# Optimization experiments

Measured on AMD Instinct MI355X. Metric: run time of the kernel, lower is better.

Reference implementation:

```python
import jax, jax.numpy as jnp
import numpy as np

N = 131072   # total nodes
G = 4096     # graphs
E = 524288   # directed bond edges
C = 96       # hidden_channels
L = 8        # num_layers
F_IN = 64    # atom features
NT = 5       # targets


def setup_inputs() -> dict:
    key = jax.random.key(0)
    ks = jax.random.split(key, 32)
    def rn(k, shape, s=0.05):
        return jax.random.normal(k, shape, jnp.float32) * s
    inp = {
        'x': jax.random.normal(ks[0], (N, F_IN), jnp.float32),
        'edge_index': jax.random.randint(ks[1], (2, E), 0, N),
        'batch': jnp.sort(jax.random.randint(ks[2], (N,), 0, G)),
        'num_graphs': G,
        # atom encoder
        'enc_w': rn(ks[3], (F_IN, C)), 'enc_b': rn(ks[4], (C,)),
        # virtual node embedding + MLP (Linear->BN->SiLU->Linear)
        'vn_emb': rn(ks[5], (C,)),
        'vn_w1': rn(ks[6], (C, C)), 'vn_b1': rn(ks[7], (C,)),
        'vn_g1': 1.0 + rn(ks[8], (C,)), 'vn_be1': rn(ks[9], (C,)),
        'vn_w2': rn(ks[10], (C, C)), 'vn_b2': rn(ks[11], (C,)),
        # per-layer GIN MLP (Linear C->2C, BN, SiLU, Linear 2C->C) stacked over L
        'conv_w1': rn(ks[12], (L, C, 2 * C)), 'conv_b1': rn(ks[13], (L, 2 * C)),
        'conv_g1': 1.0 + rn(ks[14], (L, 2 * C)), 'conv_be1': rn(ks[15], (L, 2 * C)),
        'conv_w2': rn(ks[16], (L, 2 * C, C)), 'conv_b2': rn(ks[17], (L, C)),
        # per-layer outer BatchNorm
        'bn_g': 1.0 + rn(ks[18], (L, C)), 'bn_b': rn(ks[19], (L, C)),
        # head: C->C/2 (BN,SiLU) -> C/4 (BN,SiLU) -> NT
        'h_w1': rn(ks[20], (C, C // 2)), 'h_b1': rn(ks[21], (C // 2,)),
        'h_g1': 1.0 + rn(ks[22], (C // 2,)), 'h_be1': rn(ks[23], (C // 2,)),
        'h_w2': rn(ks[24], (C // 2, C // 4)), 'h_b2': rn(ks[25], (C // 4,)),
        'h_g2': 1.0 + rn(ks[26], (C // 4,)), 'h_be2': rn(ks[27], (C // 4,)),
        'h_w3': rn(ks[28], (C // 4, NT)), 'h_b3': rn(ks[29], (NT,)),
    }
    return inp


def _bn(x, g, b, eps=1e-5):
    # training-mode BatchNorm1d: biased batch variance (matches torch normalization)
    m = x.mean(0)
    v = x.var(0)
    return (x - m) * jax.lax.rsqrt(v + eps) * g + b


def reference(x, edge_index, batch, num_graphs, enc_w, enc_b, vn_emb,
              vn_w1, vn_b1, vn_g1, vn_be1, vn_w2, vn_b2,
              conv_w1, conv_b1, conv_g1, conv_be1, conv_w2, conv_b2,
              bn_g, bn_b,
              h_w1, h_b1, h_g1, h_be1, h_w2, h_b2, h_g2, h_be2, h_w3, h_b3):
    n = x.shape[0]
    gN = int(num_graphs)
    c = enc_w.shape[1]
    nl = conv_w1.shape[0]

    h = x @ enc_w + enc_b                                   # [n, C]
    vn = jnp.broadcast_to(vn_emb, (gN, c))                  # virtual node feats
    h = jnp.concatenate([h, vn], 0)                         # [n+gN, C]

    # vectorized virtual-node edges: (n+batch[i]) <-> i, both directions
    node_ids = jnp.arange(n, dtype=batch.dtype)
    vidx = n + batch
    src = jnp.concatenate([edge_index[0], vidx, node_ids])
    tgt = jnp.concatenate([edge_index[1], node_ids, vidx])
    total = n + gN

    for i in range(nl):
        # GINConv, eps=0: MLP(x + sum_neighbors)
        agg = jax.ops.segment_sum(h[src], tgt, num_segments=total)
        z = h + agg
        z = z @ conv_w1[i] + conv_b1[i]
        z = jax.nn.silu(_bn(z, conv_g1[i], conv_be1[i]))
        z = z @ conv_w2[i] + conv_b2[i]
        z = jax.nn.silu(_bn(z, bn_g[i], bn_b[i]))           # outer BN + SiLU (dropout=eval)
        h = z if i == 0 else h + z                          # residual after layer 0
        if i < nl - 1:
            v = h[n:]
            v = jax.nn.silu(_bn(v @ vn_w1 + vn_b1, vn_g1, vn_be1)) @ vn_w2 + vn_b2
            h = jnp.concatenate([h[:n], v], 0)

    hn = h[:n]
    sums = jax.ops.segment_sum(hn, batch, num_segments=gN)
    counts = jax.ops.segment_sum(jnp.ones((n,), hn.dtype), batch, num_segments=gN)
    pooled = sums / jnp.maximum(counts, 1.0)[:, None]       # global_mean_pool

    z = jax.nn.silu(_bn(pooled @ h_w1 + h_b1, h_g1, h_be1))
    z = jax.nn.silu(_bn(z @ h_w2 + h_b2, h_g2, h_be2))
    return z @ h_w3 + h_b3                                  # [G, 5]
```

## Files before the change

### kernel.cpp

```cpp
#include <hip/hip_runtime.h>
#include <hip/hip_bf16.h>

constexpr int N_   = 131072;
constexpr int G_   = 4096;
constexpr int E_   = 524288;
constexpr int C_   = 96;
constexpr int L_   = 8;
constexpr int FIN_ = 64;
constexpr int TOT_ = N_ + G_;

typedef __attribute__((ext_vector_type(8))) short short8v;
typedef __attribute__((ext_vector_type(4))) float f32x4;
using bf16 = __hip_bfloat16;

__device__ __forceinline__ float silu_f(float y) { return y / (1.f + __expf(-y)); }
__device__ __forceinline__ float toF(float x) { return x; }
__device__ __forceinline__ float toF(bf16 x)  { return __bfloat162float(x); }
__device__ __forceinline__ float bfbits2f(short s) {
  return __uint_as_float(((unsigned)(unsigned short)s) << 16);
}
__device__ __forceinline__ short f2bfbits(float f) {
  bf16 b = __float2bfloat16(f);
  return *reinterpret_cast<short*>(&b);
}
__device__ __forceinline__ void atomAddD(double* p, double v) { unsafeAtomicAdd(p, v); }


__global__ __launch_bounds__(256) void k_cast_x(const float* __restrict__ x, bf16* __restrict__ xb) {
  int idx = blockIdx.x * 256 + threadIdx.x;
  if (idx >= N_ * FIN_) return;
  xb[idx] = __float2bfloat16(x[idx]);
}

__global__ __launch_bounds__(256) void k_transT(const float* __restrict__ src, bf16* __restrict__ dst,
                                                int Kd, int Nd, int total) {
  int idx = blockIdx.x * 256 + threadIdx.x;
  if (idx >= total) return;
  int per = Kd * Nd;
  int i   = idx / per;
  int rem = idx - i * per;
  int k   = rem / Nd;
  int n   = rem - k * Nd;
  dst[(size_t)i * per + n * Kd + k] = __float2bfloat16(src[idx]);
}

__global__ __launch_bounds__(256) void k_deg_count(const int* __restrict__ tgt, int* __restrict__ deg) {
  int e = blockIdx.x * 256 + threadIdx.x;
  if (e >= E_) return;
  atomicAdd(&deg[tgt[e]], 1);
}

__global__ __launch_bounds__(256) void k_scan_local(const int* __restrict__ deg, int* __restrict__ lp,
                                                    int* __restrict__ bsum) {
  __shared__ int s[256];
  int t = threadIdx.x;
  int i = blockIdx.x * 256 + t;
  int v = deg[i];
  s[t] = v;
  __syncthreads();
  for (int off = 1; off < 256; off <<= 1) {
    int x = (t >= off) ? s[t - off] : 0;
    __syncthreads();
    s[t] += x;
    __syncthreads();
  }
  lp[i] = s[t] - v;
  if (t == 255) bsum[blockIdx.x] = s[255];
}

__global__ __launch_bounds__(512) void k_scan_bsum(const int* __restrict__ bsum, int* __restrict__ boff) {
  __shared__ int s[512];
  int t = threadIdx.x;
  int v = bsum[t];
  s[t] = v;
  __syncthreads();
  for (int off = 1; off < 512; off <<= 1) {
    int x = (t >= off) ? s[t - off] : 0;
    __syncthreads();
    s[t] += x;
    __syncthreads();
  }
  boff[t] = s[t] - v;
}

__global__ __launch_bounds__(256) void k_scan_add(int* __restrict__ rs, const int* __restrict__ boff) {
  int i = blockIdx.x * 256 + threadIdx.x;
  if (i > N_) return;
  if (i == N_) { rs[N_] = E_; return; }
  rs[i] += boff[i >> 8];
}

__global__ __launch_bounds__(256) void k_csr_fill(const int* __restrict__ src, const int* __restrict__ tgt,
                                                  const int* __restrict__ rs, int* __restrict__ cur,
                                                  int* __restrict__ ssrc) {
  int e = blockIdx.x * 256 + threadIdx.x;
  if (e >= E_) return;
  int t = tgt[e];
  int pos = atomicAdd(&cur[t], 1);
  ssrc[rs[t] + pos] = src[e];
}

__global__ __launch_bounds__(256) void k_gbounds(const int* __restrict__ batch, int* __restrict__ gstart) {
  int i = blockIdx.x * 256 + threadIdx.x;
  if (i > N_) return;
  if (i == N_) {
    int last = batch[N_ - 1];
    for (int g = last + 1; g <= G_; ++g) gstart[g] = N_;
    return;
  }
  int b  = batch[i];
  int bp = (i == 0) ? -1 : batch[i - 1];
  for (int g = bp + 1; g <= b; ++g) gstart[g] = i;
}

__global__ __launch_bounds__(192) void k_vnagg(const bf16* __restrict__ hb, const int* __restrict__ gstart,
                                               bf16* __restrict__ vna) {
  int slot = threadIdx.x / 24;
  int c4   = (threadIdx.x % 24) * 4;
  int g = blockIdx.x * 8 + slot;
  int i0 = gstart[g], i1 = gstart[g + 1];
  float s0 = 0.f, s1 = 0.f, s2 = 0.f, s3 = 0.f;
  for (int i = i0; i < i1; ++i) {
    short4 v = *(const short4*)((const short*)hb + (size_t)i * C_ + c4);
    s0 += bfbits2f(v.x); s1 += bfbits2f(v.y); s2 += bfbits2f(v.z); s3 += bfbits2f(v.w);
  }
  short4 o;
  o.x = f2bfbits(s0); o.y = f2bfbits(s1); o.z = f2bfbits(s2); o.w = f2bfbits(s3);
  *(short4*)((short*)vna + (size_t)g * C_ + c4) = o;
}

template <int K, int NOUT, bool INACT, bool OSTATS, typename OutT>
__global__ __launch_bounds__(512) void k_gemm(const bf16* __restrict__ A, const bf16* __restrict__ Wt,
                                              const float* __restrict__ bias,
                                              const double* __restrict__ stin,
                                              const float* __restrict__ gam, const float* __restrict__ bet,
                                              float Rin,
                                              OutT* __restrict__ out, double* __restrict__ stout) {
  constexpr int KK  = K / 32;
  constexpr int NT  = NOUT / 16;
  constexpr int UPR = K / 8;
  constexpr int LPR = UPR + 1;
  constexpr int LWB  = NOUT * LPR * 16;
  constexpr int ISCB = INACT ? 2 * K * 4 : 0;
  constexpr int SMB  = LWB + (ISCB > 0 ? ISCB : 1);
  __shared__ __align__(16) char smem[SMB];
  uint4* lw   = reinterpret_cast<uint4*>(smem);
  float* lsc  = reinterpret_cast<float*>(smem + LWB);
  float* lsh  = lsc + K;
  float* ssum = reinterpret_cast<float*>(smem);
  float* sqs  = ssum + 8 * NOUT;

  const uint4* wv = (const uint4*)Wt;
  for (int u = threadIdx.x; u < NOUT * UPR; u += 512) {
    int row = u / UPR, colu = u - row * UPR;
    lw[row * LPR + colu] = wv[u];
  }
  if (INACT) {
    for (int k = threadIdx.x; k < K; k += 512) {
      double mean = stin[k] / (double)Rin;
      double var  = stin[K + k] / (double)Rin - mean * mean;
      float sc = gam[k] * rsqrtf((float)var + 1e-5f);
      lsc[k] = sc;
      lsh[k] = bet[k] - (float)mean * sc;
    }
  }
  __syncthreads();

  int wave = threadIdx.x >> 6, lane = threadIdx.x & 63;
  int m0 = (blockIdx.x * 8 + wave) * 16;
  int lr = lane & 15, lg = lane >> 4;

  short8v a[KK];
  const short* Arow = (const short*)A + (size_t)(m0 + lr) * K + lg * 8;
#pragma unroll
  for (int kk = 0; kk < KK; ++kk) {
    short8v raw = *(const short8v*)(Arow + kk * 32);
    if (INACT) {
      int kbase = kk * 32 + lg * 8;
#pragma unroll
      for (int j = 0; j < 8; ++j) {
        float f = bfbits2f(raw[j]);
        f = silu_f(fmaf(f, lsc[kbase + j], lsh[kbase + j]));
        raw[j] = f2bfbits(f);
      }
    }
    a[kk] = raw;
  }

  f32x4 acc[NT];
#pragma unroll
  for (int nt = 0; nt < NT; ++nt) acc[nt] = (f32x4){0.f, 0.f, 0.f, 0.f};

#pragma unroll
  for (int nt = 0; nt < NT; ++nt) {
    const short* brow = (const short*)&lw[(nt * 16 + lr) * LPR] + lg * 8;
#pragma unroll
    for (int kk = 0; kk < KK; ++kk) {
      short8v b = *(const short8v*)(brow + kk * 32);
      acc[nt] = __builtin_amdgcn_mfma_f32_16x16x32_bf16(a[kk], b, acc[nt], 0, 0, 0);
    }
  }

  if (OSTATS) __syncthreads();

  int orow = m0 + (lg << 2);
#pragma unroll
  for (int nt = 0; nt < NT; ++nt) {
    int col = nt * 16 + lr;
    float bi = bias[col];
    float s = 0.f, q = 0.f;
#pragma unroll
    for (int r = 0; r < 4; ++r) {
      float y = acc[nt][r] + bi;
      float yb;
      if constexpr (sizeof(OutT) == 2) {
        bf16 b = __float2bfloat16(y);
        out[(size_t)(orow + r) * NOUT + col] = b;
        yb = __bfloat162float(b);
      } else {
        out[(size_t)(orow + r) * NOUT + col] = y;
        yb = y;
      }
      if (OSTATS) { s += yb; q += yb * yb; }
    }
    if (OSTATS) {
      s += __shfl_xor(s, 16, 64); s += __shfl_xor(s, 32, 64);
      q += __shfl_xor(q, 16, 64); q += __shfl_xor(q, 32, 64);
      if (lg == 0) { ssum[wave * NOUT + col] = s; sqs[wave * NOUT + col] = q; }
    }
  }
  if (OSTATS) {
    __syncthreads();
    int tid = threadIdx.x;
    if (tid < NOUT) {
      float s = 0.f, q = 0.f;
#pragma unroll
      for (int w = 0; w < 8; ++w) { s += ssum[w * NOUT + tid]; q += sqs[w * NOUT + tid]; }
      atomAddD(&stout[tid], (double)s);
      atomAddD(&stout[NOUT + tid], (double)q);
    }
  }
}

template <int K, int NOUT>
__global__ __launch_bounds__(512) void k_gemm_agg(const bf16* __restrict__ hb,
    const int* __restrict__ batch, const int* __restrict__ rs, const int* __restrict__ ssrc,
    const bf16* __restrict__ vna, const bf16* __restrict__ Wt, const float* __restrict__ bias,
    bf16* __restrict__ out, double* __restrict__ st) {
  constexpr int KK  = K / 32;
  constexpr int NT  = NOUT / 16;
  constexpr int UPR = K / 8;
  constexpr int LPR = UPR + 1;
  constexpr int LWB = NOUT * LPR * 16;
  __shared__ __align__(16) char smem[LWB];
  uint4* lw   = reinterpret_cast<uint4*>(smem);
  float* ssum = reinterpret_cast<float*>(smem);
  float* sqs  = ssum + 8 * NOUT;

  const uint4* wv = (const uint4*)Wt;
  for (int u = threadIdx.x; u < NOUT * UPR; u += 512) {
    int row = u / UPR, colu = u - row * UPR;
    lw[row * LPR + colu] = wv[u];
  }
  __syncthreads();

  int wave = threadIdx.x >> 6, lane = threadIdx.x & 63;
  int m0 = (blockIdx.x * 8 + wave) * 16;
  int lr = lane & 15, lg = lane >> 4;
  int row = m0 + lr;
  int koff = lg * 8;

  float av[KK * 8];
#pragma unroll
  for (int t = 0; t < KK * 8; ++t) av[t] = 0.f;

  auto addPtr = [&](const short* p) {
#pragma unroll
    for (int kk = 0; kk < KK; ++kk) {
      short8v v = *(const short8v*)(p + koff + kk * 32);
#pragma unroll
      for (int j = 0; j < 8; ++j) av[kk * 8 + j] += bfbits2f(v[j]);
    }
  };
  auto addPtr2 = [&](const short* p0, const short* p1) {
    short8v v0[KK], v1[KK];
#pragma unroll
    for (int kk = 0; kk < KK; ++kk) {
      v0[kk] = *(const short8v*)(p0 + koff + kk * 32);
      v1[kk] = *(const short8v*)(p1 + koff + kk * 32);
    }
#pragma unroll
    for (int kk = 0; kk < KK; ++kk)
#pragma unroll
      for (int j = 0; j < 8; ++j)
        av[kk * 8 + j] += bfbits2f(v0[kk][j]) + bfbits2f(v1[kk][j]);
  };
  auto hrow = [&](int r) { return (const short*)hb + (size_t)r * K; };

  if (row < N_) {
    addPtr2(hrow(row), hrow(N_ + batch[row]));
    int e = rs[row], e1 = rs[row + 1];
    for (; e + 2 <= e1; e += 2) addPtr2(hrow(ssrc[e]), hrow(ssrc[e + 1]));
    if (e < e1) addPtr(hrow(ssrc[e]));
  } else {
    addPtr2(hrow(row), (const short*)vna + (size_t)(row - N_) * K);
  }

  short8v a[KK];
#pragma unroll
  for (int kk = 0; kk < KK; ++kk)
#pragma unroll
    for (int j = 0; j < 8; ++j) a[kk][j] = f2bfbits(av[kk * 8 + j]);

  f32x4 acc[NT];
#pragma unroll
  for (int nt = 0; nt < NT; ++nt) acc[nt] = (f32x4){0.f, 0.f, 0.f, 0.f};

#pragma unroll
  for (int nt = 0; nt < NT; ++nt) {
    const short* brow = (const short*)&lw[(nt * 16 + lr) * LPR] + lg * 8;
#pragma unroll
    for (int kk = 0; kk < KK; ++kk) {
      short8v b = *(const short8v*)(brow + kk * 32);
      acc[nt] = __builtin_amdgcn_mfma_f32_16x16x32_bf16(a[kk], b, acc[nt], 0, 0, 0);
    }
  }

  __syncthreads();

  int orow = m0 + (lg << 2);
#pragma unroll
  for (int nt = 0; nt < NT; ++nt) {
    int col = nt * 16 + lr;
    float bi = bias[col];
    float s = 0.f, q = 0.f;
#pragma unroll
    for (int r = 0; r < 4; ++r) {
      float y = acc[nt][r] + bi;
      bf16 b = __float2bfloat16(y);
      out[(size_t)(orow + r) * NOUT + col] = b;
      float yb = __bfloat162float(b);
      s += yb; q += yb * yb;
    }
    s += __shfl_xor(s, 16, 64); s += __shfl_xor(s, 32, 64);
    q += __shfl_xor(q, 16, 64); q += __shfl_xor(q, 32, 64);
    if (lg == 0) { ssum[wave * NOUT + col] = s; sqs[wave * NOUT + col] = q; }
  }
  __syncthreads();
  int tid = threadIdx.x;
  if (tid < NOUT) {
    float s = 0.f, q = 0.f;
#pragma unroll
    for (int w = 0; w < 8; ++w) { s += ssum[w * NOUT + tid]; q += sqs[w * NOUT + tid]; }
    atomAddD(&st[tid], (double)s);
    atomAddD(&st[NOUT + tid], (double)q);
  }
}

__global__ __launch_bounds__(256) void k_fill_vn(bf16* __restrict__ hb, const float* __restrict__ vn) {
  int idx = blockIdx.x * 256 + threadIdx.x;
  if (idx >= G_ * C_) return;
  int c = idx % C_;
  hb[(size_t)N_ * C_ + idx] = __float2bfloat16(vn[c]);
}

template <int CC, typename T>
__global__ __launch_bounds__(256) void k_bnstats(const T* __restrict__ X, int R, double* __restrict__ st) {
  int c = threadIdx.x;
  float s = 0.f, q = 0.f;
  for (int r = blockIdx.x; r < R; r += gridDim.x) {
    float v = toF(X[(size_t)r * CC + c]);
    s += v;
    q += v * v;
  }
  atomAddD(&st[c], (double)s);
  atomAddD(&st[CC + c], (double)q);
}

template <int CC>
__global__ __launch_bounds__(256) void k_bnfin(const double* __restrict__ st, int R,
    const float* __restrict__ g, const float* __restrict__ be,
    float* __restrict__ scale, float* __restrict__ shift) {
  int c = threadIdx.x;
  if (c >= CC) return;
  double mean = st[c] / R;
  double var  = st[CC + c] / R - mean * mean;
  float sc = g[c] * rsqrtf((float)var + 1e-5f);
  scale[c] = sc;
  shift[c] = be[c] - (float)mean * sc;
}

__global__ __launch_bounds__(256) void k_update(const bf16* __restrict__ Z, bf16* __restrict__ hb,
    const double* __restrict__ st,
    const float* __restrict__ gam, const float* __restrict__ bet, int addResid) {
  __shared__ float lsc[C_], lsh[C_];
  if (threadIdx.x < C_) {
    int c = threadIdx.x;
    double mean = st[c] / (double)TOT_;
    double var  = st[C_ + c] / (double)TOT_ - mean * mean;
    float sc = gam[c] * rsqrtf((float)var + 1e-5f);
    lsc[c] = sc;
    lsh[c] = bet[c] - (float)mean * sc;
  }
  __syncthreads();
  int idx = blockIdx.x * 256 + threadIdx.x;
  if (idx >= TOT_ * C_ / 8) return;
  int cg = idx % (C_ / 8);
  int c0 = cg * 8;
  short8v zv = ((const short8v*)Z)[idx];
  short8v hv = ((const short8v*)hb)[idx];
  short8v o;
#pragma unroll
  for (int j = 0; j < 8; ++j) {
    float y = silu_f(fmaf(bfbits2f(zv[j]), lsc[c0 + j], lsh[c0 + j]));
    float hn = addResid ? (bfbits2f(hv[j]) + y) : y;
    o[j] = f2bfbits(hn);
  }
  ((short8v*)hb)[idx] = o;
}

template <int K, int M, bool INACT>
__global__ __launch_bounds__(256) void k_mm(const float* __restrict__ A,
    const float* __restrict__ W, const float* __restrict__ bias,
    const float* __restrict__ isc, const float* __restrict__ ish,
    float* __restrict__ out, int R) {
  int idx = blockIdx.x * 256 + threadIdx.x;
  if (idx >= R * M) return;
  int row = idx / M;
  int m   = idx - row * M;
  const float* ar = A + (size_t)row * K;
  float s = bias[m];
#pragma unroll 8
  for (int k = 0; k < K; ++k) {
    float a = ar[k];
    if (INACT) a = silu_f(fmaf(a, isc[k], ish[k]));
    s = fmaf(a, W[k * M + m], s);
  }
  out[idx] = s;
}

__global__ __launch_bounds__(256) void k_pool2(const bf16* __restrict__ hb, const int* __restrict__ gstart,
                                               float* __restrict__ pooled) {
  int idx = blockIdx.x * 256 + threadIdx.x;
  if (idx >= G_ * C_) return;
  int g = idx / C_;
  int c = idx - g * C_;
  int i0 = gstart[g], i1 = gstart[g + 1];
  float s = 0.f;
  for (int i = i0; i < i1; ++i) s += toF(hb[(size_t)i * C_ + c]);
  pooled[idx] = s / fmaxf((float)(i1 - i0), 1.0f);
}

static inline int gblk(long n) { return (int)((n + 255) / 256); }

extern "C" void kernel_launch(void* const* d_in, const int* in_sizes, int n_in,
                              void* d_out, int out_size, void* d_ws, size_t ws_size,
                              hipStream_t stream) {
  (void)in_sizes; (void)n_in; (void)out_size; (void)ws_size;
  const float* x       = (const float*)d_in[0];
  const int*   ei      = (const int*)d_in[1];
  const int*   batch   = (const int*)d_in[2];
  const float* enc_w   = (const float*)d_in[4];
  const float* enc_b   = (const float*)d_in[5];
  const float* vn_emb  = (const float*)d_in[6];
  const float* vn_w1   = (const float*)d_in[7];
  const float* vn_b1   = (const float*)d_in[8];
  const float* vn_g1   = (const float*)d_in[9];
  const float* vn_be1  = (const float*)d_in[10];
  const float* vn_w2   = (const float*)d_in[11];
  const float* vn_b2   = (const float*)d_in[12];
  const float* conv_w1 = (const float*)d_in[13];
  const float* conv_b1 = (const float*)d_in[14];
  const float* conv_g1 = (const float*)d_in[15];
  const float* conv_be1= (const float*)d_in[16];
  const float* conv_w2 = (const float*)d_in[17];
  const float* conv_b2 = (const float*)d_in[18];
  const float* bn_g    = (const float*)d_in[19];
  const float* bn_b    = (const float*)d_in[20];
  const float* h_w1    = (const float*)d_in[21];
  const float* h_b1    = (const float*)d_in[22];
  const float* h_g1    = (const float*)d_in[23];
  const float* h_be1   = (const float*)d_in[24];
  const float* h_w2    = (const float*)d_in[25];
  const float* h_b2    = (const float*)d_in[26];
  const float* h_g2    = (const float*)d_in[27];
  const float* h_be2   = (const float*)d_in[28];
  const float* h_w3    = (const float*)d_in[29];
  const float* h_b3    = (const float*)d_in[30];
  float* out = (float*)d_out;

  const int* e_src = ei;
  const int* e_tgt = ei + E_;

  char* p = (char*)d_ws;
  auto alloc = [&](size_t bytes) -> char* {
    char* r = p;
    p += (bytes + 15) & ~size_t(15);
    return r;
  };
  bf16*   hbf    = (bf16*)  alloc((size_t)TOT_ * C_ * 2);
  bf16*   vna    = (bf16*)  alloc((size_t)G_ * C_ * 2);
  bf16*   vtb    = (bf16*)  alloc((size_t)G_ * C_ * 2);
  float*  pooled = (float*) alloc((size_t)G_ * C_ * 4);
  float*  t1     = (float*) alloc((size_t)G_ * 48 * 4);
  float*  t2     = (float*) alloc((size_t)G_ * 24 * 4);
  float*  scale1 = (float*) alloc(256 * 4);
  float*  shift1 = (float*) alloc(256 * 4);
  float*  scale2 = (float*) alloc(256 * 4);
  float*  shift2 = (float*) alloc(256 * 4);
  double* stbuf  = (double*)alloc((size_t)26 * 384 * 8);
  bf16*   z1     = (bf16*)  alloc((size_t)TOT_ * 2 * C_ * 2);
  bf16*   z2     = (bf16*)  alloc((size_t)TOT_ * C_ * 2);
  bf16*   xb     = (bf16*)  alloc((size_t)N_ * FIN_ * 2);
  bf16*   encwT  = (bf16*)  alloc((size_t)C_ * FIN_ * 2);
  bf16*   w1T    = (bf16*)  alloc((size_t)L_ * 2 * C_ * C_ * 2);
  bf16*   w2T    = (bf16*)  alloc((size_t)L_ * C_ * 2 * C_ * 2);
  bf16*   vnw1T  = (bf16*)  alloc((size_t)C_ * C_ * 2);
  bf16*   vnw2T  = (bf16*)  alloc((size_t)C_ * C_ * 2);
  int*    deg    = (int*)   alloc((size_t)N_ * 4);
  int*    cur    = (int*)   alloc((size_t)N_ * 4);
  int*    rs     = (int*)   alloc((size_t)(N_ + 1) * 4);
  int*    bsum   = (int*)   alloc(512 * 4);
  int*    boff   = (int*)   alloc(512 * 4);
  int*    ssrc   = (int*)   alloc((size_t)E_ * 4);
  int*    gstart = (int*)   alloc((size_t)(G_ + 1) * 4);

  auto ST = [&](int i) { return stbuf + (size_t)i * 384; };

  k_cast_x<<<gblk((long)N_ * FIN_), 256, 0, stream>>>(x, xb);
  k_transT<<<gblk((long)FIN_ * C_), 256, 0, stream>>>(enc_w, encwT, FIN_, C_, FIN_ * C_);
  k_transT<<<gblk((long)L_ * C_ * 2 * C_), 256, 0, stream>>>(conv_w1, w1T, C_, 2 * C_, L_ * C_ * 2 * C_);
  k_transT<<<gblk((long)L_ * 2 * C_ * C_), 256, 0, stream>>>(conv_w2, w2T, 2 * C_, C_, L_ * 2 * C_ * C_);
  k_transT<<<gblk((long)C_ * C_), 256, 0, stream>>>(vn_w1, vnw1T, C_, C_, C_ * C_);
  k_transT<<<gblk((long)C_ * C_), 256, 0, stream>>>(vn_w2, vnw2T, C_, C_, C_ * C_);

  hipMemsetAsync(deg, 0, (size_t)N_ * 4, stream);
  hipMemsetAsync(cur, 0, (size_t)N_ * 4, stream);
  hipMemsetAsync(stbuf, 0, (size_t)26 * 384 * 8, stream);
  k_deg_count<<<gblk(E_), 256, 0, stream>>>(e_tgt, deg);
  k_scan_local<<<N_ / 256, 256, 0, stream>>>(deg, rs, bsum);
  k_scan_bsum<<<1, 512, 0, stream>>>(bsum, boff);
  k_scan_add<<<gblk(N_ + 1), 256, 0, stream>>>(rs, boff);
  k_csr_fill<<<gblk(E_), 256, 0, stream>>>(e_src, e_tgt, rs, cur, ssrc);
  k_gbounds<<<gblk(N_ + 1), 256, 0, stream>>>(batch, gstart);

  k_gemm<FIN_, C_, false, false, bf16><<<N_ / 128, 512, 0, stream>>>(
      xb, encwT, enc_b, nullptr, nullptr, nullptr, 1.f, hbf, nullptr);
  k_fill_vn<<<gblk((long)G_ * C_), 256, 0, stream>>>(hbf, vn_emb);

  for (int i = 0; i < L_; ++i) {
    const bf16*  wt1 = w1T + (size_t)i * 2 * C_ * C_;
    const bf16*  wt2 = w2T + (size_t)i * C_ * 2 * C_;
    const float* b1  = conv_b1 + (size_t)i * 2 * C_;
    const float* g1  = conv_g1 + (size_t)i * 2 * C_;
    const float* be1 = conv_be1+ (size_t)i * 2 * C_;
    const float* b2  = conv_b2 + (size_t)i * C_;
    const float* bg  = bn_g    + (size_t)i * C_;
    const float* bb  = bn_b    + (size_t)i * C_;

    k_vnagg<<<G_ / 8, 192, 0, stream>>>(hbf, gstart, vna);

    k_gemm_agg<C_, 2 * C_><<<TOT_ / 128, 512, 0, stream>>>(
        hbf, batch, rs, ssrc, vna, wt1, b1, z1, ST(i));

    k_gemm<2 * C_, C_, true, true, bf16><<<TOT_ / 128, 512, 0, stream>>>(
        z1, wt2, b2, ST(i), g1, be1, (float)TOT_, z2, ST(8 + i));

    k_update<<<(int)((long)TOT_ * C_ / 8 / 256), 256, 0, stream>>>(z2, hbf, ST(8 + i), bg, bb, i > 0);

    if (i < L_ - 1) {
      k_gemm<C_, C_, false, true, bf16><<<G_ / 128, 512, 0, stream>>>(
          hbf + (size_t)N_ * C_, vnw1T, vn_b1, nullptr, nullptr, nullptr, 1.f, vtb, ST(16 + i));
      k_gemm<C_, C_, true, false, bf16><<<G_ / 128, 512, 0, stream>>>(
          vtb, vnw2T, vn_b2, ST(16 + i), vn_g1, vn_be1, (float)G_,
          hbf + (size_t)N_ * C_, nullptr);
    }
  }

  k_pool2<<<gblk((long)G_ * C_), 256, 0, stream>>>(hbf, gstart, pooled);

  k_mm<C_, 48, false><<<gblk((long)G_ * 48), 256, 0, stream>>>(
      pooled, h_w1, h_b1, nullptr, nullptr, t1, G_);
  k_bnstats<48, float><<<64, 48, 0, stream>>>(t1, G_, ST(23));
  k_bnfin<48><<<1, 48, 0, stream>>>(ST(23), G_, h_g1, h_be1, scale1, shift1);

  k_mm<48, 24, true><<<gblk((long)G_ * 24), 256, 0, stream>>>(
      t1, h_w2, h_b2, scale1, shift1, t2, G_);
  k_bnstats<24, float><<<64, 24, 0, stream>>>(t2, G_, ST(24));
  k_bnfin<24><<<1, 24, 0, stream>>>(ST(24), G_, h_g2, h_be2, scale2, shift2);

  k_mm<24, 5, true><<<gblk((long)G_ * 5), 256, 0, stream>>>(
      t2, h_w3, h_b3, scale2, shift2, out, G_);
}
```

Baseline: 1.267 ms.

## Fuse x cast into encoder GEMM, merge weight transposes, add nontemporal accesses

The separate fp32-to-bf16 cast of x is removed, and the encoder GEMM now reads fp32 x directly and converts it in registers. The six weight-transpose launches are merged into one k_prep kernel. Nontemporal loads and stores are added on the z1/z2 streaming paths, and the barrier after weight staging is moved after the A-tile global loads so they overlap the LDS fill. Together these cut launches and one full pass over x, at the cost of reading fp32 x at twice the bytes inside the GEMM.

Result: slower. 1.440 ms (+13.6%).

```diff
diff --git a/kernel.cpp b/kernel.cpp
--- a/kernel.cpp
+++ b/kernel.cpp
@@ -25,23 +25,27 @@
 }
 __device__ __forceinline__ void atomAddD(double* p, double v) { unsafeAtomicAdd(p, v); }
 
-
-__global__ __launch_bounds__(256) void k_cast_x(const float* __restrict__ x, bf16* __restrict__ xb) {
+static inline int gblk(long n) { return (int)((n + 255) / 256); }
+
+__global__ __launch_bounds__(256) void k_prep(const float* __restrict__ enc_w,
+    const float* __restrict__ conv_w1, const float* __restrict__ conv_w2,
+    const float* __restrict__ vn_w1, const float* __restrict__ vn_w2,
+    bf16* __restrict__ encwT, bf16* __restrict__ w1T, bf16* __restrict__ w2T,
+    bf16* __restrict__ vnw1T, bf16* __restrict__ vnw2T) {
   int idx = blockIdx.x * 256 + threadIdx.x;
-  if (idx >= N_ * FIN_) return;
-  xb[idx] = __float2bfloat16(x[idx]);
-}
-
-__global__ __launch_bounds__(256) void k_transT(const float* __restrict__ src, bf16* __restrict__ dst,
-                                                int Kd, int Nd, int total) {
-  int idx = blockIdx.x * 256 + threadIdx.x;
-  if (idx >= total) return;
+  const float* src; bf16* dst; int Kd, Nd, local;
+  if (idx < 6144)        { src = enc_w;   dst = encwT; Kd = 64;  Nd = 96;  local = idx; }
+  else if (idx < 153600) { src = conv_w1; dst = w1T;   Kd = 96;  Nd = 192; local = idx - 6144; }
+  else if (idx < 301056) { src = conv_w2; dst = w2T;   Kd = 192; Nd = 96;  local = idx - 153600; }
+  else if (idx < 310272) { src = vn_w1;   dst = vnw1T; Kd = 96;  Nd = 96;  local = idx - 301056; }
+  else if (idx < 319488) { src = vn_w2;   dst = vnw2T; Kd = 96;  Nd = 96;  local = idx - 310272; }
+  else return;
   int per = Kd * Nd;
-  int i   = idx / per;
-  int rem = idx - i * per;
+  int i   = local / per;
+  int rem = local - i * per;
   int k   = rem / Nd;
   int n   = rem - k * Nd;
-  dst[(size_t)i * per + n * Kd + k] = __float2bfloat16(src[idx]);
+  dst[(size_t)i * per + n * Kd + k] = __float2bfloat16(src[local]);
 }
 
 __global__ __launch_bounds__(256) void k_deg_count(const int* __restrict__ tgt, int* __restrict__ deg) {
@@ -129,8 +133,8 @@
   *(short4*)((short*)vna + (size_t)g * C_ + c4) = o;
 }
 
-template <int K, int NOUT, bool INACT, bool OSTATS, typename OutT>
-__global__ __launch_bounds__(512) void k_gemm(const bf16* __restrict__ A, const bf16* __restrict__ Wt,
+template <int K, int NOUT, bool INACT, bool OSTATS, bool AF32, bool NTA, bool NTO, typename OutT>
+__global__ __launch_bounds__(512) void k_gemm(const void* __restrict__ Aptr, const bf16* __restrict__ Wt,
                                               const float* __restrict__ bias,
                                               const double* __restrict__ stin,
                                               const float* __restrict__ gam, const float* __restrict__ bet,
@@ -164,27 +168,45 @@
       lsh[k] = bet[k] - (float)mean * sc;
     }
   }
-  __syncthreads();
 
   int wave = threadIdx.x >> 6, lane = threadIdx.x & 63;
   int m0 = (blockIdx.x * 8 + wave) * 16;
   int lr = lane & 15, lg = lane >> 4;
 
   short8v a[KK];
-  const short* Arow = (const short*)A + (size_t)(m0 + lr) * K + lg * 8;
-#pragma unroll
-  for (int kk = 0; kk < KK; ++kk) {
-    short8v raw = *(const short8v*)(Arow + kk * 32);
-    if (INACT) {
+  if constexpr (AF32) {
+    const float* Arow = (const float*)Aptr + (size_t)(m0 + lr) * K + lg * 8;
+#pragma unroll
+    for (int kk = 0; kk < KK; ++kk) {
+      float4 f0 = *(const float4*)(Arow + kk * 32);
+      float4 f1 = *(const float4*)(Arow + kk * 32 + 4);
+      a[kk][0] = f2bfbits(f0.x); a[kk][1] = f2bfbits(f0.y);
+      a[kk][2] = f2bfbits(f0.z); a[kk][3] = f2bfbits(f0.w);
+      a[kk][4] = f2bfbits(f1.x); a[kk][5] = f2bfbits(f1.y);
+      a[kk][6] = f2bfbits(f1.z); a[kk][7] = f2bfbits(f1.w);
+    }
+  } else {
+    const short* Arow = (const short*)Aptr + (size_t)(m0 + lr) * K + lg * 8;
+#pragma unroll
+    for (int kk = 0; kk < KK; ++kk) {
+      if constexpr (NTA) a[kk] = __builtin_nontemporal_load((const short8v*)(Arow + kk * 32));
+      else               a[kk] = *(const short8v*)(Arow + kk * 32);
+    }
+  }
+
+  __syncthreads();
+
+  if (INACT) {
+#pragma unroll
+    for (int kk = 0; kk < KK; ++kk) {
       int kbase = kk * 32 + lg * 8;
 #pragma unroll
       for (int j = 0; j < 8; ++j) {
-        float f = bfbits2f(raw[j]);
+        float f = bfbits2f(a[kk][j]);
         f = silu_f(fmaf(f, lsc[kbase + j], lsh[kbase + j]));
-        raw[j] = f2bfbits(f);
+        a[kk][j] = f2bfbits(f);
       }
     }
-    a[kk] = raw;
   }
 
   f32x4 acc[NT];
@@ -213,12 +235,15 @@
     for (int r = 0; r < 4; ++r) {
       float y = acc[nt][r] + bi;
       float yb;
+      size_t off = (size_t)(orow + r) * NOUT + col;
       if constexpr (sizeof(OutT) == 2) {
-        bf16 b = __float2bfloat16(y);
-        out[(size_t)(orow + r) * NOUT + col] = b;
-        yb = __bfloat162float(b);
+        short bits = f2bfbits(y);
+        if constexpr (NTO) __builtin_nontemporal_store(bits, (short*)out + off);
+        else               ((short*)out)[off] = bits;
+        yb = bfbits2f(bits);
       } else {
-        out[(size_t)(orow + r) * NOUT + col] = y;
+        if constexpr (NTO) __builtin_nontemporal_store(y, (float*)out + off);
+        else               ((float*)out)[off] = y;
         yb = y;
       }
       if (OSTATS) { s += yb; q += yb * yb; }
@@ -262,7 +287,6 @@
     int row = u / UPR, colu = u - row * UPR;
     lw[row * LPR + colu] = wv[u];
   }
-  __syncthreads();
 
   int wave = threadIdx.x >> 6, lane = threadIdx.x & 63;
   int m0 = (blockIdx.x * 8 + wave) * 16;
@@ -312,6 +336,8 @@
 #pragma unroll
     for (int j = 0; j < 8; ++j) a[kk][j] = f2bfbits(av[kk * 8 + j]);
 
+  __syncthreads();
+
   f32x4 acc[NT];
 #pragma unroll
   for (int nt = 0; nt < NT; ++nt) acc[nt] = (f32x4){0.f, 0.f, 0.f, 0.f};
@@ -337,9 +363,9 @@
 #pragma unroll
     for (int r = 0; r < 4; ++r) {
       float y = acc[nt][r] + bi;
-      bf16 b = __float2bfloat16(y);
-      out[(size_t)(orow + r) * NOUT + col] = b;
-      float yb = __bfloat162float(b);
+      short bits = f2bfbits(y);
+      __builtin_nontemporal_store(bits, (short*)out + (size_t)(orow + r) * NOUT + col);
+      float yb = bfbits2f(bits);
       s += yb; q += yb * yb;
     }
     s += __shfl_xor(s, 16, 64); s += __shfl_xor(s, 32, 64);
@@ -407,7 +433,7 @@
   if (idx >= TOT_ * C_ / 8) return;
   int cg = idx % (C_ / 8);
   int c0 = cg * 8;
-  short8v zv = ((const short8v*)Z)[idx];
+  short8v zv = __builtin_nontemporal_load((const short8v*)Z + idx);
   short8v hv = ((const short8v*)hb)[idx];
   short8v o;
 #pragma unroll
@@ -450,8 +476,6 @@
   for (int i = i0; i < i1; ++i) s += toF(hb[(size_t)i * C_ + c]);
   pooled[idx] = s / fmaxf((float)(i1 - i0), 1.0f);
 }
-
-static inline int gblk(long n) { return (int)((n + 255) / 256); }
 
 extern "C" void kernel_launch(void* const* d_in, const int* in_sizes, int n_in,
                               void* d_out, int out_size, void* d_ws, size_t ws_size,
@@ -511,7 +535,6 @@
   double* stbuf  = (double*)alloc((size_t)26 * 384 * 8);
   bf16*   z1     = (bf16*)  alloc((size_t)TOT_ * 2 * C_ * 2);
   bf16*   z2     = (bf16*)  alloc((size_t)TOT_ * C_ * 2);
-  bf16*   xb     = (bf16*)  alloc((size_t)N_ * FIN_ * 2);
   bf16*   encwT  = (bf16*)  alloc((size_t)C_ * FIN_ * 2);
   bf16*   w1T    = (bf16*)  alloc((size_t)L_ * 2 * C_ * C_ * 2);
   bf16*   w2T    = (bf16*)  alloc((size_t)L_ * C_ * 2 * C_ * 2);
@@ -527,12 +550,8 @@
 
   auto ST = [&](int i) { return stbuf + (size_t)i * 384; };
 
-  k_cast_x<<<gblk((long)N_ * FIN_), 256, 0, stream>>>(x, xb);
-  k_transT<<<gblk((long)FIN_ * C_), 256, 0, stream>>>(enc_w, encwT, FIN_, C_, FIN_ * C_);
-  k_transT<<<gblk((long)L_ * C_ * 2 * C_), 256, 0, stream>>>(conv_w1, w1T, C_, 2 * C_, L_ * C_ * 2 * C_);
-  k_transT<<<gblk((long)L_ * 2 * C_ * C_), 256, 0, stream>>>(conv_w2, w2T, 2 * C_, C_, L_ * 2 * C_ * C_);
-  k_transT<<<gblk((long)C_ * C_), 256, 0, stream>>>(vn_w1, vnw1T, C_, C_, C_ * C_);
-  k_transT<<<gblk((long)C_ * C_), 256, 0, stream>>>(vn_w2, vnw2T, C_, C_, C_ * C_);
+  k_prep<<<gblk(319488), 256, 0, stream>>>(enc_w, conv_w1, conv_w2, vn_w1, vn_w2,
+                                           encwT, w1T, w2T, vnw1T, vnw2T);
 
   hipMemsetAsync(deg, 0, (size_t)N_ * 4, stream);
   hipMemsetAsync(cur, 0, (size_t)N_ * 4, stream);
@@ -544,8 +563,8 @@
   k_csr_fill<<<gblk(E_), 256, 0, stream>>>(e_src, e_tgt, rs, cur, ssrc);
   k_gbounds<<<gblk(N_ + 1), 256, 0, stream>>>(batch, gstart);
 
-  k_gemm<FIN_, C_, false, false, bf16><<<N_ / 128, 512, 0, stream>>>(
-      xb, encwT, enc_b, nullptr, nullptr, nullptr, 1.f, hbf, nullptr);
+  k_gemm<FIN_, C_, false, false, true, false, false, bf16><<<N_ / 128, 512, 0, stream>>>(
+      x, encwT, enc_b, nullptr, nullptr, nullptr, 1.f, hbf, nullptr);
   k_fill_vn<<<gblk((long)G_ * C_), 256, 0, stream>>>(hbf, vn_emb);
 
   for (int i = 0; i < L_; ++i) {
@@ -563,15 +582,15 @@
     k_gemm_agg<C_, 2 * C_><<<TOT_ / 128, 512, 0, stream>>>(
         hbf, batch, rs, ssrc, vna, wt1, b1, z1, ST(i));
 
-    k_gemm<2 * C_, C_, true, true, bf16><<<TOT_ / 128, 512, 0, stream>>>(
+    k_gemm<2 * C_, C_, true, true, false, true, true, bf16><<<TOT_ / 128, 512, 0, stream>>>(
         z1, wt2, b2, ST(i), g1, be1, (float)TOT_, z2, ST(8 + i));
 
     k_update<<<(int)((long)TOT_ * C_ / 8 / 256), 256, 0, stream>>>(z2, hbf, ST(8 + i), bg, bb, i > 0);
 
     if (i < L_ - 1) {
-      k_gemm<C_, C_, false, true, bf16><<<G_ / 128, 512, 0, stream>>>(
+      k_gemm<C_, C_, false, true, false, false, false, bf16><<<G_ / 128, 512, 0, stream>>>(
           hbf + (size_t)N_ * C_, vnw1T, vn_b1, nullptr, nullptr, nullptr, 1.f, vtb, ST(16 + i));
-      k_gemm<C_, C_, true, false, bf16><<<G_ / 128, 512, 0, stream>>>(
+      k_gemm<C_, C_, true, false, false, false, false, bf16><<<G_ / 128, 512, 0, stream>>>(
           vtb, vnw2T, vn_b2, ST(16 + i), vn_g1, vn_be1, (float)G_,
           hbf + (size_t)N_ * C_, nullptr);
     }
```
